# Kernel optimization log

Measured on AMD Instinct MI355X. Metric: run time of the kernel, lower is better.

Reference implementation:

```python
import jax, jax.numpy as jnp
import numpy as np

HIDDEN_DIM = 128
NUM_HEADS = 4
B, S = 16, 1024
NEG = -1e9
EPS = 1e-5


def setup_inputs() -> dict:
    key = jax.random.key(0)
    ks = jax.random.split(key, 6)
    D, H = HIDDEN_DIM, NUM_HEADS
    x = jax.random.normal(ks[0], (B, S, D), dtype=jnp.float32)
    edge_type_matrix = jax.random.randint(ks[1], (S, S), 0, 5, dtype=jnp.int64)
    scale = 0.02
    W_in = jax.random.normal(ks[2], (H, 3 * D, D), dtype=jnp.float32) * scale   # per-head in_proj_weight
    b_in = jax.random.normal(ks[3], (H, 3 * D), dtype=jnp.float32) * scale      # per-head in_proj_bias
    W_out = jax.random.normal(ks[4], (H, D, D), dtype=jnp.float32) * scale      # per-head out_proj.weight
    b_out = jax.random.normal(ks[5], (H, D), dtype=jnp.float32) * scale         # per-head out_proj.bias
    return {"x": x, "edge_type_matrix": edge_type_matrix,
            "W_in": W_in, "b_in": b_in, "W_out": W_out, "b_out": b_out}


def reference(x, edge_type_matrix, W_in, b_in, W_out, b_out):
    Bx, Sx, D = x.shape
    H = W_in.shape[0]
    # F.layer_norm(x, x.size()[1:]): normalize jointly over (S, D), no affine
    mu = jnp.mean(x, axis=(1, 2), keepdims=True)
    var = jnp.mean(jnp.square(x - mu), axis=(1, 2), keepdims=True)
    xn = (x - mu) / jnp.sqrt(var + EPS)
    # all heads' qkv in one contraction: [b,h,s,3D]
    qkv = jnp.einsum('bsd,hed->bhse', xn, W_in) + b_in[None, :, None, :]
    q, k, v = jnp.split(qkv, 3, axis=-1)                      # each [b,h,s,D]
    scores = jnp.einsum('bhsd,bhtd->bhst', q, k) / jnp.sqrt(jnp.float32(D))
    # additive mask per head: 0 where edge_type == head_id(1..H), else -1e9
    head_ids = jnp.arange(1, H + 1, dtype=edge_type_matrix.dtype)
    mask = jnp.where(edge_type_matrix[None, :, :] == head_ids[:, None, None],
                     jnp.float32(0.0), jnp.float32(NEG))       # [h,s,s]
    attn = jax.nn.softmax(scores + mask[None], axis=-1)
    ctx = jnp.einsum('bhst,bhtd->bhsd', attn, v)
    # torch out_proj: ctx @ W.T + b
    out_h = jnp.einsum('bhsd,hed->bhse', ctx, W_out) + b_out[None, :, None, :]
    # dropout p=0.05 is identity in eval mode; concat heads on feature dim
    out = jnp.transpose(out_h, (0, 2, 1, 3)).reshape(Bx, Sx, H * D)
    return out


if __name__ == '__main__':
    inp = setup_inputs()
    y = reference(**inp)
    print(y.shape)
```

## Files before the change

kernel.cpp:

```cpp
#include <hip/hip_runtime.h>
#include <math.h>

static constexpr int Dh = 128;
static constexpr int NH = 4;
static constexpr int NB = 16;
static constexpr int SS = 1024;
static constexpr float NEGF = -1e9f;
static constexpr float SCALE = 0.08838834764831843f;

typedef short s16x8 __attribute__((ext_vector_type(8)));
typedef short s16x4 __attribute__((ext_vector_type(4)));
typedef float f32x4 __attribute__((ext_vector_type(4)));

#define MFMA32(a, b, c) __builtin_amdgcn_mfma_f32_16x16x32_bf16(a, b, c, 0, 0, 0)
#define MFMA16(a, b, c) __builtin_amdgcn_mfma_f32_16x16x16bf16_1k(a, b, c, 0, 0, 0)

__device__ inline ushort f2bf(float f) {
    union { float f; unsigned u; } v; v.f = f;
    unsigned r = v.u + 0x7FFFu + ((v.u >> 16) & 1u);
    return (ushort)(r >> 16);
}

__global__ __launch_bounds__(256) void ln_mask_kernel(const float* __restrict__ x,
                                                      float* __restrict__ part,
                                                      const int* __restrict__ edge,
                                                      unsigned long long* __restrict__ mbit) {
    const int b = blockIdx.x >> 4, p = blockIdx.x & 15;
    const int tid = threadIdx.x;
    const float4* xb = (const float4*)(x + (size_t)b * SS * Dh) + p * 2048;
    float s = 0.f, ss = 0.f;
    for (int i = tid; i < 2048; i += 256) {
        float4 v = xb[i];
        s  += v.x + v.y + v.z + v.w;
        ss += v.x * v.x + v.y * v.y + v.z * v.z + v.w * v.w;
    }
    __shared__ float r1[256], r2[256];
    r1[tid] = s; r2[tid] = ss;
    __syncthreads();
    for (int off = 128; off > 0; off >>= 1) {
        if (tid < off) { r1[tid] += r1[tid + off]; r2[tid] += r2[tid + off]; }
        __syncthreads();
    }
    if (tid == 0) { part[blockIdx.x * 2] = r1[0]; part[blockIdx.x * 2 + 1] = r2[0]; }

    if (blockIdx.x < 64) {
        const int idx = blockIdx.x * 256 + tid;
        const int sr = idx >> 4, w = idx & 15;
        const int4* ep = (const int4*)(edge + (size_t)sr * SS + w * 64);
        unsigned long long m0 = 0, m1 = 0, m2 = 0, m3 = 0;
        #pragma unroll
        for (int j = 0; j < 16; ++j) {
            int4 e = ep[j];
            const int base = j * 4;
            m0 |= (e.x == 1) ? (1ull << (base + 0)) : 0ull;
            m1 |= (e.x == 2) ? (1ull << (base + 0)) : 0ull;
            m2 |= (e.x == 3) ? (1ull << (base + 0)) : 0ull;
            m3 |= (e.x == 4) ? (1ull << (base + 0)) : 0ull;
            m0 |= (e.y == 1) ? (1ull << (base + 1)) : 0ull;
            m1 |= (e.y == 2) ? (1ull << (base + 1)) : 0ull;
            m2 |= (e.y == 3) ? (1ull << (base + 1)) : 0ull;
            m3 |= (e.y == 4) ? (1ull << (base + 1)) : 0ull;
            m0 |= (e.z == 1) ? (1ull << (base + 2)) : 0ull;
            m1 |= (e.z == 2) ? (1ull << (base + 2)) : 0ull;
            m2 |= (e.z == 3) ? (1ull << (base + 2)) : 0ull;
            m3 |= (e.z == 4) ? (1ull << (base + 2)) : 0ull;
            m0 |= (e.w == 1) ? (1ull << (base + 3)) : 0ull;
            m1 |= (e.w == 2) ? (1ull << (base + 3)) : 0ull;
            m2 |= (e.w == 3) ? (1ull << (base + 3)) : 0ull;
            m3 |= (e.w == 4) ? (1ull << (base + 3)) : 0ull;
        }
        mbit[((size_t)0 * SS + sr) * 16 + w] = m0;
        mbit[((size_t)1 * SS + sr) * 16 + w] = m1;
        mbit[((size_t)2 * SS + sr) * 16 + w] = m2;
        mbit[((size_t)3 * SS + sr) * 16 + w] = m3;
    }
}

__global__ __launch_bounds__(256) void qkv_mfma_kernel(const float* __restrict__ x,
                                                       const float* __restrict__ w,
                                                       const float* __restrict__ bias,
                                                       const float* __restrict__ part,
                                                       ushort* __restrict__ qo,
                                                       ushort* __restrict__ ko,
                                                       ushort* __restrict__ vto) {
    __shared__ ushort smem[2 * 128 * 72];
    ushort* As = smem;
    ushort* Bs = smem + 128 * 72;
    ushort* Rs = smem;
    const int tid = threadIdx.x, wave = tid >> 6, lane = tid & 63;
    const int lrow = lane & 15, quad = lane >> 4;
    const int wm = wave & 1, wn = wave >> 1;
    const int col0 = blockIdx.x * 128;
    const int row0 = blockIdx.y * 128;
    const int bb = row0 >> 10;

    float s_ = 0.f, ss_ = 0.f;
    #pragma unroll
    for (int p = 0; p < 16; ++p) { s_ += part[(bb * 16 + p) * 2]; ss_ += part[(bb * 16 + p) * 2 + 1]; }
    const float invN = 1.0f / (float)(SS * Dh);
    const float mu = s_ * invN;
    const float rstd = 1.0f / sqrtf(ss_ * invN - mu * mu + 1e-5f);

    f32x4 acc[4][4];
    #pragma unroll
    for (int mi = 0; mi < 4; ++mi)
        #pragma unroll
        for (int ni = 0; ni < 4; ++ni) acc[mi][ni] = (f32x4){0.f, 0.f, 0.f, 0.f};

    for (int kk = 0; kk < 128; kk += 64) {
        if (kk) __syncthreads();
        #pragma unroll
        for (int p = 0; p < 8; ++p) {
            int slot = p * 256 + tid;
            int r = slot >> 4, c4 = (slot & 15) << 2;
            float4 v = *(const float4*)(x + (size_t)(row0 + r) * Dh + kk + c4);
            ushort4 pa;
            pa.x = f2bf((v.x - mu) * rstd); pa.y = f2bf((v.y - mu) * rstd);
            pa.z = f2bf((v.z - mu) * rstd); pa.w = f2bf((v.w - mu) * rstd);
            *(ushort4*)&As[r * 72 + c4] = pa;
            float4 wv = *(const float4*)(w + (size_t)(col0 + r) * Dh + kk + c4);
            ushort4 pb;
            pb.x = f2bf(wv.x); pb.y = f2bf(wv.y); pb.z = f2bf(wv.z); pb.w = f2bf(wv.w);
            *(ushort4*)&Bs[r * 72 + c4] = pb;
        }
        __syncthreads();
        #pragma unroll
        for (int kc = 0; kc < 2; ++kc) {
            s16x8 af[4], bf[4];
            #pragma unroll
            for (int mi = 0; mi < 4; ++mi)
                af[mi] = *(const s16x8*)&As[(wm * 64 + 16 * mi + lrow) * 72 + kc * 32 + quad * 8];
            #pragma unroll
            for (int ni = 0; ni < 4; ++ni)
                bf[ni] = *(const s16x8*)&Bs[(wn * 64 + 16 * ni + lrow) * 72 + kc * 32 + quad * 8];
            #pragma unroll
            for (int mi = 0; mi < 4; ++mi)
                #pragma unroll
                for (int ni = 0; ni < 4; ++ni)
                    acc[mi][ni] = MFMA32(af[mi], bf[ni], acc[mi][ni]);
        }
    }

    const int seg = col0 % 384, typ = seg >> 7, h = col0 / 384;
    const size_t bh = (size_t)bb * NH + h;
    const int sl_blk = row0 & 1023;
    float bia[4];
    #pragma unroll
    for (int ni = 0; ni < 4; ++ni) bia[ni] = bias[col0 + wn * 64 + 16 * ni + lrow];
    const float sc = (typ == 0) ? SCALE : 1.f;

    __syncthreads();
    if (typ < 2) {
        #pragma unroll
        for (int mi = 0; mi < 4; ++mi)
            #pragma unroll
            for (int ni = 0; ni < 4; ++ni)
                #pragma unroll
                for (int reg = 0; reg < 4; ++reg)
                    Rs[(wm * 64 + 16 * mi + quad * 4 + reg) * 136 + wn * 64 + 16 * ni + lrow]
                        = f2bf((acc[mi][ni][reg] + bia[ni]) * sc);
    } else {
        #pragma unroll
        for (int mi = 0; mi < 4; ++mi)
            #pragma unroll
            for (int ni = 0; ni < 4; ++ni) {
                ushort4 pk;
                pk.x = f2bf(acc[mi][ni][0] + bia[ni]);
                pk.y = f2bf(acc[mi][ni][1] + bia[ni]);
                pk.z = f2bf(acc[mi][ni][2] + bia[ni]);
                pk.w = f2bf(acc[mi][ni][3] + bia[ni]);
                *(ushort4*)&Rs[(wn * 64 + 16 * ni + lrow) * 136 + wm * 64 + 16 * mi + quad * 4] = pk;
            }
    }
    __syncthreads();

    ushort* dstb;
    int pitch;
    if (typ == 0)      { dstb = qo  + bh * SS * 128 + (size_t)sl_blk * 128; pitch = 128; }
    else if (typ == 1) { dstb = ko  + bh * SS * 128 + (size_t)sl_blk * 128; pitch = 128; }
    else               { dstb = vto + bh * (size_t)128 * SS + sl_blk;       pitch = SS;  }
    #pragma unroll
    for (int p = 0; p < 8; ++p) {
        int slot = p * 256 + tid;
        int r = slot >> 4, c8 = (slot & 15) * 8;
        *(s16x8*)&dstb[(size_t)r * pitch + c8] = *(const s16x8*)&Rs[r * 136 + c8];
    }
}

static constexpr int KS_LD = 136;
static constexpr int VT_LD = 72;
static constexpr int WS_LD = 136;
static constexpr int OS_LD = 136;
static constexpr int SMEM_N = 26112;

__global__ __launch_bounds__(256, 2) void attn_fused_kernel(const ushort* __restrict__ qg_,
                                                            const ushort* __restrict__ kg_,
                                                            const ushort* __restrict__ vg_,
                                                            const unsigned long long* __restrict__ mbit,
                                                            const float* __restrict__ wo,
                                                            const float* __restrict__ bo,
                                                            float* __restrict__ out) {
    const int bhi = blockIdx.x, qt = blockIdx.y;
    const int b = bhi >> 2, h = bhi & 3;
    const int s0 = qt * 128;
    const int tid = threadIdx.x;
    const int wave = tid >> 6, lane = tid & 63;
    const int lrow = lane & 15, quad = lane >> 4;

    __shared__ ushort smem[SMEM_N];
    ushort* Ks  = smem;
    ushort* Vt  = smem + 64 * KS_LD;
    ushort* Osl = smem + wave * 16 * OS_LD;
    ushort* Ws  = smem + 4 * 16 * OS_LD;

    const size_t bh = (size_t)(b * NH + h);
    const ushort* qg = qg_ + bh * SS * 128;
    const ushort* kg = kg_ + bh * SS * 128;
    const ushort* vg = vg_ + bh * 128 * SS;
    const unsigned long long* mrow0 = mbit + ((size_t)h * SS + (s0 + 32 * wave + lrow)) * 16;
    const unsigned long long* mrow1 = mrow0 + 16 * 16;

    s16x8 qf[2][4];
    #pragma unroll
    for (int g = 0; g < 2; ++g) {
        const ushort* qr = qg + (size_t)(s0 + 32 * wave + 16 * g + lrow) * 128 + quad * 8;
        #pragma unroll
        for (int kc = 0; kc < 4; ++kc) qf[g][kc] = *(const s16x8*)(qr + kc * 32);
    }

    s16x8 kreg[4], vreg[4];
    #pragma unroll
    for (int p = 0; p < 4; ++p) {
        int slot = p * 256 + tid;
        int r = slot >> 4, c = (slot & 15) * 8;
        kreg[p] = *(const s16x8*)(kg + (size_t)r * 128 + c);
    }
    #pragma unroll
    for (int p = 0; p < 4; ++p) {
        int slot = p * 256 + tid;
        int r = slot >> 3, c = (slot & 7) * 8;
        vreg[p] = *(const s16x8*)(vg + (size_t)r * SS + c);
    }

    f32x4 oacc[2][8];
    #pragma unroll
    for (int g = 0; g < 2; ++g)
        #pragma unroll
        for (int nb = 0; nb < 8; ++nb) oacc[g][nb] = (f32x4){0.f, 0.f, 0.f, 0.f};
    float m_run[2] = {-INFINITY, -INFINITY};
    float l_run[2] = {0.f, 0.f};

    for (int kt = 0; kt < 16; ++kt) {
        const int t0 = kt * 64;
        unsigned long long mw0 = mrow0[kt];
        unsigned long long mw1 = mrow1[kt];

        __syncthreads();
        #pragma unroll
        for (int p = 0; p < 4; ++p) {
            int slot = p * 256 + tid;
            int r = slot >> 4, c = (slot & 15) * 8;
            *(s16x8*)&Ks[r * KS_LD + c] = kreg[p];
        }
        #pragma unroll
        for (int p = 0; p < 4; ++p) {
            int slot = p * 256 + tid;
            int r = slot >> 3, c = (slot & 7) * 8;
            *(s16x8*)&Vt[r * VT_LD + c] = vreg[p];
        }
        __syncthreads();

        if (kt < 15) {
            const int t1 = t0 + 64;
            #pragma unroll
            for (int p = 0; p < 4; ++p) {
                int slot = p * 256 + tid;
                int r = slot >> 4, c = (slot & 15) * 8;
                kreg[p] = *(const s16x8*)(kg + (size_t)(t1 + r) * 128 + c);
            }
            #pragma unroll
            for (int p = 0; p < 4; ++p) {
                int slot = p * 256 + tid;
                int r = slot >> 3, c = (slot & 7) * 8;
                vreg[p] = *(const s16x8*)(vg + (size_t)r * SS + t1 + c);
            }
        }

        f32x4 sacc[2][4];
        #pragma unroll
        for (int g = 0; g < 2; ++g)
            #pragma unroll
            for (int cb = 0; cb < 4; ++cb) sacc[g][cb] = (f32x4){0.f, 0.f, 0.f, 0.f};
        #pragma unroll
        for (int cb = 0; cb < 4; ++cb) {
            s16x8 kf[4];
            #pragma unroll
            for (int kc = 0; kc < 4; ++kc)
                kf[kc] = *(const s16x8*)&Ks[(16 * cb + lrow) * KS_LD + kc * 32 + quad * 8];
            #pragma unroll
            for (int g = 0; g < 2; ++g)
                #pragma unroll
                for (int kc = 0; kc < 4; ++kc)
                    sacc[g][cb] = MFMA32(kf[kc], qf[g][kc], sacc[g][cb]);
        }

        s16x4 pf[2][4];
        #pragma unroll
        for (int g = 0; g < 2; ++g) {
            const unsigned long long mw = g ? mw1 : mw0;
            float sv[4][4];
            float tm = -INFINITY;
            #pragma unroll
            for (int cb = 0; cb < 4; ++cb) {
                unsigned nib = (unsigned)(mw >> (16 * cb + quad * 4)) & 0xFu;
                #pragma unroll
                for (int r = 0; r < 4; ++r) {
                    sv[cb][r] = (nib & (1u << r)) ? sacc[g][cb][r] : NEGF;
                    tm = fmaxf(tm, sv[cb][r]);
                }
            }
            tm = fmaxf(tm, __shfl_xor(tm, 16));
            tm = fmaxf(tm, __shfl_xor(tm, 32));
            float mn = fmaxf(m_run[g], tm);
            float al = __expf(m_run[g] - mn);
            float rs = 0.f;
            #pragma unroll
            for (int cb = 0; cb < 4; ++cb) {
                float p0 = __expf(sv[cb][0] - mn);
                float p1 = __expf(sv[cb][1] - mn);
                float p2 = __expf(sv[cb][2] - mn);
                float p3 = __expf(sv[cb][3] - mn);
                rs += (p0 + p1) + (p2 + p3);
                s16x4 pk;
                pk[0] = (short)f2bf(p0); pk[1] = (short)f2bf(p1);
                pk[2] = (short)f2bf(p2); pk[3] = (short)f2bf(p3);
                pf[g][cb] = pk;
            }
            rs += __shfl_xor(rs, 16);
            rs += __shfl_xor(rs, 32);
            l_run[g] = l_run[g] * al + rs;
            m_run[g] = mn;
            #pragma unroll
            for (int nb = 0; nb < 8; ++nb)
                #pragma unroll
                for (int r = 0; r < 4; ++r) oacc[g][nb][r] *= al;
        }

        #pragma unroll
        for (int nb = 0; nb < 8; ++nb) {
            #pragma unroll
            for (int kb = 0; kb < 4; ++kb) {
                s16x4 vf = *(const s16x4*)&Vt[(16 * nb + lrow) * VT_LD + kb * 16 + quad * 4];
                #pragma unroll
                for (int g = 0; g < 2; ++g)
                    oacc[g][nb] = MFMA16(vf, pf[g][kb], oacc[g][nb]);
            }
        }
    }

    __syncthreads();
    const float* wbase = wo + (size_t)h * Dh * Dh;
    #pragma unroll
    for (int p = 0; p < 16; ++p) {
        int slot = p * 256 + tid;
        int r = slot >> 5, c4 = (slot & 31) << 2;
        float4 wv = *(const float4*)(wbase + (size_t)r * Dh + c4);
        ushort4 pb;
        pb.x = f2bf(wv.x); pb.y = f2bf(wv.y); pb.z = f2bf(wv.z); pb.w = f2bf(wv.w);
        *(ushort4*)&Ws[r * WS_LD + c4] = pb;
    }
    s16x8 afo[2][4];
    #pragma unroll
    for (int g = 0; g < 2; ++g) {
        float inv = 1.0f / l_run[g];
        #pragma unroll
        for (int nb = 0; nb < 8; ++nb) {
            ushort4 pk;
            pk.x = f2bf(oacc[g][nb][0] * inv);
            pk.y = f2bf(oacc[g][nb][1] * inv);
            pk.z = f2bf(oacc[g][nb][2] * inv);
            pk.w = f2bf(oacc[g][nb][3] * inv);
            *(ushort4*)&Osl[lrow * OS_LD + 16 * nb + quad * 4] = pk;
        }
        #pragma unroll
        for (int kc = 0; kc < 4; ++kc)
            afo[g][kc] = *(const s16x8*)&Osl[lrow * OS_LD + kc * 32 + quad * 8];
    }
    __syncthreads();

    const size_t orow0 = (size_t)b * SS + s0 + 32 * wave;
    #pragma unroll
    for (int nb = 0; nb < 8; ++nb) {
        float bia = bo[h * Dh + nb * 16 + lrow];
        f32x4 facc[2];
        facc[0] = (f32x4){0.f, 0.f, 0.f, 0.f};
        facc[1] = (f32x4){0.f, 0.f, 0.f, 0.f};
        #pragma unroll
        for (int kc = 0; kc < 4; ++kc) {
            s16x8 wf = *(const s16x8*)&Ws[(16 * nb + lrow) * WS_LD + kc * 32 + quad * 8];
            facc[0] = MFMA32(afo[0][kc], wf, facc[0]);
            facc[1] = MFMA32(afo[1][kc], wf, facc[1]);
        }
        #pragma unroll
        for (int g = 0; g < 2; ++g)
            #pragma unroll
            for (int reg = 0; reg < 4; ++reg) {
                size_t m = orow0 + 16 * g + quad * 4 + reg;
                out[m * (NH * Dh) + h * Dh + nb * 16 + lrow] = facc[g][reg] + bia;
            }
    }
}

extern "C" void kernel_launch(void* const* d_in, const int* in_sizes, int n_in,
                              void* d_out, int out_size, void* d_ws, size_t ws_size,
                              hipStream_t stream) {
    const float* x     = (const float*)d_in[0];
    const int*   edge  = (const int*)d_in[1];
    const float* w_in  = (const float*)d_in[2];
    const float* b_in  = (const float*)d_in[3];
    const float* w_out = (const float*)d_in[4];
    const float* b_out = (const float*)d_in[5];
    float* out = (float*)d_out;

    float* ws   = (float*)d_ws;
    float* part = ws;
    unsigned long long* mbit = (unsigned long long*)(ws + 1024);
    ushort* qo  = (ushort*)(mbit + (size_t)NH * SS * 16);
    const size_t QSZ = (size_t)NB * NH * SS * 128;
    ushort* ko  = qo + QSZ;
    ushort* vto = ko + QSZ;

    ln_mask_kernel<<<256, 256, 0, stream>>>(x, part, edge, mbit);
    qkv_mfma_kernel<<<dim3(12, 128), 256, 0, stream>>>(x, w_in, b_in, part, qo, ko, vto);
    attn_fused_kernel<<<dim3(NB * NH, SS / 128), 256, 0, stream>>>(qo, ko, vto, mbit, w_out, b_out, out);
}
```

Measured before the change: 175.6 us.

## Pre-cast normalized x and W_in to bf16 before the QKV GEMM

Adds a separate xcast kernel that applies the layer-norm statistics and writes x as bf16, and converts W_in to bf16 inside spare blocks of the LN/mask kernel. The QKV GEMM then loads bf16 tiles directly into shared memory instead of loading fp32 and normalizing and converting per tile. Before, each x tile was converted 12 times (once per column block) and each weight tile 128 times. The change adds one kernel launch and an extra write and read of a bf16 copy of x through the workspace.

```diff
diff --git a/kernel.cpp b/kernel.cpp
--- a/kernel.cpp
+++ b/kernel.cpp
@@ -24,13 +24,15 @@
 __global__ __launch_bounds__(256) void ln_mask_kernel(const float* __restrict__ x,
                                                       float* __restrict__ part,
                                                       const int* __restrict__ edge,
-                                                      unsigned long long* __restrict__ mbit) {
+                                                      unsigned long long* __restrict__ mbit,
+                                                      const float* __restrict__ w_in,
+                                                      ushort* __restrict__ wb) {
     const int b = blockIdx.x >> 4, p = blockIdx.x & 15;
     const int tid = threadIdx.x;
-    const float4* xb = (const float4*)(x + (size_t)b * SS * Dh) + p * 2048;
+    const float4* xb4 = (const float4*)(x + (size_t)b * SS * Dh) + p * 2048;
     float s = 0.f, ss = 0.f;
     for (int i = tid; i < 2048; i += 256) {
-        float4 v = xb[i];
+        float4 v = xb4[i];
         s  += v.x + v.y + v.z + v.w;
         ss += v.x * v.x + v.y * v.y + v.z * v.z + v.w * v.w;
     }
@@ -73,13 +75,43 @@
         mbit[((size_t)1 * SS + sr) * 16 + w] = m1;
         mbit[((size_t)2 * SS + sr) * 16 + w] = m2;
         mbit[((size_t)3 * SS + sr) * 16 + w] = m3;
-    }
-}
-
-__global__ __launch_bounds__(256) void qkv_mfma_kernel(const float* __restrict__ x,
-                                                       const float* __restrict__ w,
+    } else if (blockIdx.x < 160) {
+        const int slot = (blockIdx.x - 64) * 256 + tid;
+        const float4* sp = (const float4*)w_in + (size_t)slot * 2;
+        float4 a = sp[0], c = sp[1];
+        s16x8 pk;
+        pk[0] = (short)f2bf(a.x); pk[1] = (short)f2bf(a.y);
+        pk[2] = (short)f2bf(a.z); pk[3] = (short)f2bf(a.w);
+        pk[4] = (short)f2bf(c.x); pk[5] = (short)f2bf(c.y);
+        pk[6] = (short)f2bf(c.z); pk[7] = (short)f2bf(c.w);
+        *(s16x8*)(wb + (size_t)slot * 8) = pk;
+    }
+}
+
+__global__ __launch_bounds__(256) void xcast_kernel(const float* __restrict__ x,
+                                                    const float* __restrict__ part,
+                                                    ushort* __restrict__ xb) {
+    const int b = blockIdx.x >> 6;
+    float s = 0.f, ss = 0.f;
+    #pragma unroll
+    for (int p = 0; p < 16; ++p) { s += part[(b * 16 + p) * 2]; ss += part[(b * 16 + p) * 2 + 1]; }
+    const float invN = 1.0f / (float)(SS * Dh);
+    const float mu = s * invN;
+    const float rstd = 1.0f / sqrtf(ss * invN - mu * mu + 1e-5f);
+    const size_t base = ((size_t)blockIdx.x * 256 + threadIdx.x) * 8;
+    float4 v0 = *(const float4*)(x + base);
+    float4 v1 = *(const float4*)(x + base + 4);
+    s16x8 pk;
+    pk[0] = (short)f2bf((v0.x - mu) * rstd); pk[1] = (short)f2bf((v0.y - mu) * rstd);
+    pk[2] = (short)f2bf((v0.z - mu) * rstd); pk[3] = (short)f2bf((v0.w - mu) * rstd);
+    pk[4] = (short)f2bf((v1.x - mu) * rstd); pk[5] = (short)f2bf((v1.y - mu) * rstd);
+    pk[6] = (short)f2bf((v1.z - mu) * rstd); pk[7] = (short)f2bf((v1.w - mu) * rstd);
+    *(s16x8*)(xb + base) = pk;
+}
+
+__global__ __launch_bounds__(256) void qkv_mfma_kernel(const ushort* __restrict__ xb,
+                                                       const ushort* __restrict__ wb,
                                                        const float* __restrict__ bias,
-                                                       const float* __restrict__ part,
                                                        ushort* __restrict__ qo,
                                                        ushort* __restrict__ ko,
                                                        ushort* __restrict__ vto) {
@@ -94,13 +126,6 @@
     const int row0 = blockIdx.y * 128;
     const int bb = row0 >> 10;
 
-    float s_ = 0.f, ss_ = 0.f;
-    #pragma unroll
-    for (int p = 0; p < 16; ++p) { s_ += part[(bb * 16 + p) * 2]; ss_ += part[(bb * 16 + p) * 2 + 1]; }
-    const float invN = 1.0f / (float)(SS * Dh);
-    const float mu = s_ * invN;
-    const float rstd = 1.0f / sqrtf(ss_ * invN - mu * mu + 1e-5f);
-
     f32x4 acc[4][4];
     #pragma unroll
     for (int mi = 0; mi < 4; ++mi)
@@ -110,18 +135,11 @@
     for (int kk = 0; kk < 128; kk += 64) {
         if (kk) __syncthreads();
         #pragma unroll
-        for (int p = 0; p < 8; ++p) {
+        for (int p = 0; p < 4; ++p) {
             int slot = p * 256 + tid;
-            int r = slot >> 4, c4 = (slot & 15) << 2;
-            float4 v = *(const float4*)(x + (size_t)(row0 + r) * Dh + kk + c4);
-            ushort4 pa;
-            pa.x = f2bf((v.x - mu) * rstd); pa.y = f2bf((v.y - mu) * rstd);
-            pa.z = f2bf((v.z - mu) * rstd); pa.w = f2bf((v.w - mu) * rstd);
-            *(ushort4*)&As[r * 72 + c4] = pa;
-            float4 wv = *(const float4*)(w + (size_t)(col0 + r) * Dh + kk + c4);
-            ushort4 pb;
-            pb.x = f2bf(wv.x); pb.y = f2bf(wv.y); pb.z = f2bf(wv.z); pb.w = f2bf(wv.w);
-            *(ushort4*)&Bs[r * 72 + c4] = pb;
+            int r = slot >> 3, c8 = (slot & 7) * 8;
+            *(s16x8*)&As[r * 72 + c8] = *(const s16x8*)(xb + (size_t)(row0 + r) * Dh + kk + c8);
+            *(s16x8*)&Bs[r * 72 + c8] = *(const s16x8*)(wb + (size_t)(col0 + r) * Dh + kk + c8);
         }
         __syncthreads();
         #pragma unroll
@@ -429,8 +447,11 @@
     const size_t QSZ = (size_t)NB * NH * SS * 128;
     ushort* ko  = qo + QSZ;
     ushort* vto = ko + QSZ;
-
-    ln_mask_kernel<<<256, 256, 0, stream>>>(x, part, edge, mbit);
-    qkv_mfma_kernel<<<dim3(12, 128), 256, 0, stream>>>(x, w_in, b_in, part, qo, ko, vto);
+    ushort* xb  = vto + QSZ;
+    ushort* wb  = xb + (size_t)NB * SS * Dh;
+
+    ln_mask_kernel<<<256, 256, 0, stream>>>(x, part, edge, mbit, w_in, wb);
+    xcast_kernel<<<1024, 256, 0, stream>>>(x, part, xb);
+    qkv_mfma_kernel<<<dim3(12, 128), 256, 0, stream>>>(xb, wb, b_in, qo, ko, vto);
     attn_fused_kernel<<<dim3(NB * NH, SS / 128), 256, 0, stream>>>(qo, ko, vto, mbit, w_out, b_out, out);
 }
```

Measured after the change: 164.9 us. 1.07x faster.
